# Performance work log

Measured on AMD Instinct MI355X. Metric: run time of the kernel, lower is better.

## Reference

```python
import jax, jax.numpy as jnp
import numpy as np

D = 512       # hidden_size (attention defaults hardcode 512)
N = 8         # num_heads
H = D // N    # depth per head = 64
FF = 2048     # FFN filter size (hardcoded)
EPS = 1e-6


def _layer_norm(x, gamma, beta):
    # matches functional layer_norm: biased variance, eps inside sqrt
    mean = jnp.mean(x, axis=-1, keepdims=True)
    var = jnp.mean((x - mean) ** 2, axis=-1, keepdims=True)
    return gamma * ((x - mean) / jnp.sqrt(var + EPS)) + beta


def setup_inputs() -> dict:
    key = jax.random.key(0)
    ks = jax.random.split(key, 12)
    B, S = 8, 1024
    s = lambda k, shape, scale: jax.random.normal(k, shape, jnp.float32) * scale
    return {
        "inputs": s(ks[0], (B, S, D), 1.0),
        "attention_bias": jnp.zeros((B, 1, 1, S), jnp.float32),
        "ln1_g": jnp.ones((D,), jnp.float32),
        "ln1_b": jnp.zeros((D,), jnp.float32),
        "wq": s(ks[1], (D, N, H), D ** -0.5),
        "wk": s(ks[2], (D, N, H), D ** -0.5),
        "wv": s(ks[3], (D, N, H), D ** -0.5),
        "wo": s(ks[4], (N, H, D), D ** -0.5),
        "ln2_g": jnp.ones((D,), jnp.float32),
        "ln2_b": jnp.zeros((D,), jnp.float32),
        "w1": s(ks[5], (D, FF), D ** -0.5),
        "b1": jnp.zeros((FF,), jnp.float32),
        "w2": s(ks[6], (FF, D), FF ** -0.5),
        "b2": jnp.zeros((D,), jnp.float32),
    }


def reference(inputs, attention_bias, ln1_g, ln1_b, wq, wk, wv, wo,
              ln2_g, ln2_b, w1, b1, w2, b2):
    # --- self-attention block (pre-LN, residual) ---
    y = _layer_norm(inputs, ln1_g, ln1_b)
    q = jnp.einsum('bsd,dnh->bsnh', y, wq) * (H ** -0.5)
    k = jnp.einsum('bsd,dnh->bsnh', y, wk)
    v = jnp.einsum('bsd,dnh->bsnh', y, wv)
    # logits[b,n,f,t] = sum_h k[b,t,n,h] * q[b,f,n,h]
    logits = jnp.einsum('btnh,bfnh->bnft', k, q) + attention_bias
    weights = jax.nn.softmax(logits, axis=3)
    attn = jnp.einsum('bnft,btnh->bfnh', weights, v)
    attn_out = jnp.einsum('bfnh,nhd->bfd', attn, wo)
    x = inputs + attn_out

    # --- FFN block (pre-LN, residual) ---
    y2 = _layer_norm(x, ln2_g, ln2_b)
    h = jax.nn.relu(jnp.einsum('bsd,df->bsf', y2, w1) + b1)
    ffn_out = jnp.einsum('bsf,fd->bsd', h, w2) + b2
    return x + ffn_out
```

## Files before the change

kernel.cpp:

```cpp
#include <hip/hip_runtime.h>
#include <stdint.h>

typedef unsigned short u16;
typedef __attribute__((ext_vector_type(8))) __bf16 bf16x8;
typedef __attribute__((ext_vector_type(2))) __bf16 bf16x2;
typedef __attribute__((ext_vector_type(4))) float f32x4;

__device__ __forceinline__ float bf2f(u16 u) {
    union { unsigned int i; float f; } c; c.i = ((unsigned int)u) << 16; return c.f;
}
__device__ __forceinline__ u16 f2bf_sw(float f) {
    union { float f; unsigned int i; } c; c.f = f;
    unsigned int u = c.i;
    u += 0x7FFFu + ((u >> 16) & 1u);
    return (u16)(u >> 16);
}
__device__ __forceinline__ unsigned f2bf2(float lo, float hi) {
#if __has_builtin(__builtin_amdgcn_cvt_pk_bf16_f32)
    union { bf16x2 v; unsigned u; } c;
    c.v = __builtin_amdgcn_cvt_pk_bf16_f32(lo, hi);
    return c.u;
#else
    return (unsigned)f2bf_sw(lo) | ((unsigned)f2bf_sw(hi) << 16);
#endif
}
__device__ __forceinline__ u16 f2bf(float f) {
#if __has_builtin(__builtin_amdgcn_cvt_pk_bf16_f32)
    return (u16)(f2bf2(f, 0.f) & 0xFFFFu);
#else
    return f2bf_sw(f);
#endif
}
__device__ __forceinline__ bool sniff_f32(const unsigned* probe) {
    return probe && ((*probe & 0xFFFFu) == 0u);
}
__device__ __forceinline__ float lde(const void* p, size_t i, bool isf32) {
    return isf32 ? ((const float*)p)[i] : bf2f(((const u16*)p)[i]);
}
__device__ __forceinline__ void g2lds16(const void* g, void* l) {
    __builtin_amdgcn_global_load_lds(
        (__attribute__((address_space(1))) void*)(uintptr_t)g,
        (__attribute__((address_space(3))) void*)(unsigned int)(uintptr_t)l,
        16, 0, 0);
}

__global__ void prep_weights(const void* __restrict__ wq, const void* __restrict__ wk,
                             const void* __restrict__ wv, const void* __restrict__ wo,
                             const void* __restrict__ w1, const void* __restrict__ w2,
                             u16* __restrict__ wqkvT, u16* __restrict__ woT,
                             u16* __restrict__ w1T, u16* __restrict__ w2T,
                             const unsigned* probe) {
    __shared__ u16 t[32][33];
    const bool isf32 = sniff_f32(probe);
    const int id = blockIdx.x;
    const void* src; u16* dst; int R, C, cb, rb; float scale = 1.f;
    if (id < 1024) {
        const int which = id >> 8, tl = id & 255;
        R = 512; C = 512; cb = (tl & 15) * 32; rb = (tl >> 4) * 32;
        if (which == 0)      { src = wq; dst = wqkvT;              scale = 0.18033688011112042f; }
        else if (which == 1) { src = wk; dst = wqkvT + 512 * 512; }
        else if (which == 2) { src = wv; dst = wqkvT + 1024 * 512; }
        else                 { src = wo; dst = woT; }
    } else if (id < 2048) {
        const int tl = id - 1024; src = w1; dst = w1T; R = 512; C = 2048;
        cb = (tl & 63) * 32; rb = (tl >> 6) * 32;
    } else {
        const int tl = id - 2048; src = w2; dst = w2T; R = 2048; C = 512;
        cb = (tl & 15) * 32; rb = (tl >> 4) * 32;
    }
    const int tx = threadIdx.x, ty = threadIdx.y;
#pragma unroll
    for (int i = 0; i < 4; i++)
        t[ty + i * 8][tx] = f2bf(lde(src, (size_t)(rb + ty + i * 8) * C + cb + tx, isf32));
    __syncthreads();
#pragma unroll
    for (int i = 0; i < 4; i++) {
        float v = bf2f(t[tx][ty + i * 8]) * scale;
        dst[(size_t)(cb + ty + i * 8) * R + rb + tx] = f2bf(v);
    }
}

__global__ __launch_bounds__(256) void ln_any(const void* __restrict__ x,
                                              const void* __restrict__ gw,
                                              const void* __restrict__ bw,
                                              u16* __restrict__ y,
                                              const unsigned* probe_x,
                                              const unsigned* probe_gb) {
    const bool xf32 = sniff_f32(probe_x);
    const bool gf32 = sniff_f32(probe_gb);
    const int lane = threadIdx.x & 63, wave = threadIdx.x >> 6;
    const int r = blockIdx.x * 4 + wave;
    union U8 { uint4 v; u16 s[8]; };
    float xs[8];
    if (xf32) {
        const float4* xr = (const float4*)((const float*)x + (size_t)r * 512 + lane * 8);
        float4 p0 = xr[0], p1 = xr[1];
        xs[0]=p0.x; xs[1]=p0.y; xs[2]=p0.z; xs[3]=p0.w;
        xs[4]=p1.x; xs[5]=p1.y; xs[6]=p1.z; xs[7]=p1.w;
    } else {
        U8 xu; xu.v = *(const uint4*)((const u16*)x + (size_t)r * 512 + lane * 8);
#pragma unroll
        for (int j = 0; j < 8; j++) xs[j] = bf2f(xu.s[j]);
    }
    float s1 = 0.f, s2 = 0.f;
#pragma unroll
    for (int j = 0; j < 8; j++) { s1 += xs[j]; s2 += xs[j] * xs[j]; }
#pragma unroll
    for (int d = 1; d < 64; d <<= 1) { s1 += __shfl_xor(s1, d); s2 += __shfl_xor(s2, d); }
    const float mean = s1 * (1.f / 512.f);
    const float var = s2 * (1.f / 512.f) - mean * mean;
    const float rstd = rsqrtf(var + 1e-6f);
    float gs[8], bs[8];
    if (gf32) {
        const float4* gr = (const float4*)((const float*)gw + lane * 8);
        const float4* br = (const float4*)((const float*)bw + lane * 8);
        float4 g0 = gr[0], g1 = gr[1], b0 = br[0], b1 = br[1];
        gs[0]=g0.x; gs[1]=g0.y; gs[2]=g0.z; gs[3]=g0.w; gs[4]=g1.x; gs[5]=g1.y; gs[6]=g1.z; gs[7]=g1.w;
        bs[0]=b0.x; bs[1]=b0.y; bs[2]=b0.z; bs[3]=b0.w; bs[4]=b1.x; bs[5]=b1.y; bs[6]=b1.z; bs[7]=b1.w;
    } else {
        U8 gu; gu.v = *(const uint4*)((const u16*)gw + lane * 8);
        U8 bu; bu.v = *(const uint4*)((const u16*)bw + lane * 8);
#pragma unroll
        for (int j = 0; j < 8; j++) { gs[j] = bf2f(gu.s[j]); bs[j] = bf2f(bu.s[j]); }
    }
    uint4 ov;
    float o[8];
#pragma unroll
    for (int j = 0; j < 8; j++) o[j] = gs[j] * ((xs[j] - mean) * rstd) + bs[j];
    ov.x = f2bf2(o[0], o[1]); ov.y = f2bf2(o[2], o[3]);
    ov.z = f2bf2(o[4], o[5]); ov.w = f2bf2(o[6], o[7]);
    *(uint4*)(y + (size_t)r * 512 + lane * 8) = ov;
}

template <int EPI, int TM>
__global__ __launch_bounds__(256, 2) void gemm_bt(const u16* __restrict__ A,
                                                  const u16* __restrict__ Bt,
                                                  const void* __restrict__ bias,
                                                  const void* __restrict__ res,
                                                  void* __restrict__ out,
                                                  u16* __restrict__ out2,
                                                  const unsigned* probe,
                                                  int M, int N, int K) {
    constexpr int ACH = TM / 16;
    constexpr int MI = TM / 32;
    __shared__ __align__(16) u16 lA[2][TM * 32];
    __shared__ __align__(16) u16 lB[2][128 * 32];
    const int tid = threadIdx.x, wave = tid >> 6, lane = tid & 63;
    const int m0 = blockIdx.x * TM, n0 = blockIdx.y * 128;
    const int wm = (wave >> 1) * (TM / 2), wn = (wave & 1) * 64;
    const int row = lane & 15, quad = lane >> 4;
    f32x4 acc[MI][4];
#pragma unroll
    for (int i = 0; i < MI; i++)
#pragma unroll
        for (int j = 0; j < 4; j++) acc[i][j] = (f32x4){0.f, 0.f, 0.f, 0.f};
    const u16* Ab = A + (size_t)m0 * K;
    const u16* Bb = Bt + (size_t)n0 * K;

    auto stage = [&](int buf, int k0) {
#pragma unroll
        for (int c = 0; c < (ACH + 8 + 3) / 4; c++) {
            const int ch = c * 4 + wave;
            if (ch < ACH) {
                const int e = ch * 64 + lane;
                const int r = e >> 2, col = (e & 3) * 8;
                g2lds16(Ab + (size_t)r * K + k0 + col, (char*)lA[buf] + ch * 1024);
            } else if (ch < ACH + 8) {
                const int c2 = ch - ACH;
                const int e = c2 * 64 + lane;
                const int r = e >> 2, col = (e & 3) * 8;
                g2lds16(Bb + (size_t)r * K + k0 + col, (char*)lB[buf] + c2 * 1024);
            }
        }
    };

    stage(0, 0);
    int cur = 0;
    for (int k0 = 0; k0 < K; k0 += 32) {
        __syncthreads();
        if (k0 + 32 < K) stage(cur ^ 1, k0 + 32);
        bf16x8 af[MI], bfr[4];
#pragma unroll
        for (int t = 0; t < MI; t++)
            af[t]  = *(const bf16x8*)(lA[cur] + (wm + t * 16 + row) * 32 + quad * 8);
#pragma unroll
        for (int t = 0; t < 4; t++)
            bfr[t] = *(const bf16x8*)(lB[cur] + (wn + t * 16 + row) * 32 + quad * 8);
#pragma unroll
        for (int i = 0; i < MI; i++)
#pragma unroll
            for (int j = 0; j < 4; j++)
                acc[i][j] = __builtin_amdgcn_mfma_f32_16x16x32_bf16(af[i], bfr[j], acc[i][j], 0, 0, 0);
        cur ^= 1;
    }
    const bool isf32 = sniff_f32(probe);
#pragma unroll
    for (int i = 0; i < MI; i++) {
        const int gm = m0 + wm + i * 16 + quad * 4;
#pragma unroll
        for (int j = 0; j < 4; j++) {
            const int gn = n0 + wn + j * 16 + row;
            float bv = 0.f;
            if (EPI == 2 || EPI == 3) bv = lde(bias, gn, isf32);
#pragma unroll
            for (int r = 0; r < 4; r++) {
                float v = acc[i][j][r];
                const int gmr = gm + r;
                size_t idx = (size_t)gmr * N + gn;
                if (EPI == 1) {
                    ((u16*)out)[idx] = f2bf(v + lde(res, idx, isf32));
                } else if (EPI == 2) {
                    v += bv;
                    ((u16*)out)[idx] = f2bf(v > 0.f ? v : 0.f);
                } else if (EPI == 3) {
                    v += bv + bf2f(((const u16*)res)[idx]);
                    if (isf32) ((float*)out)[idx] = v;
                    else       ((u16*)out)[idx] = f2bf(v);
                } else {
                    if (gn < 1024) {
                        ((u16*)out)[(size_t)gmr * 1024 + gn] = f2bf(v);
                    } else {
                        const int j2 = gn - 1024, n = j2 >> 6, h2 = j2 & 63;
                        const int b = gmr >> 10, t = gmr & 1023;
                        const int ut = t & 31, vt = ut & 15;
                        const int tP = (t & ~31) | ((vt >> 2) * 8 + ((ut >> 4) << 2) + (vt & 3));
                        out2[(((size_t)b * 8 + n) * 64 + h2) * 1024 + tP] = f2bf(v);
                    }
                }
            }
        }
    }
}

__global__ __launch_bounds__(256, 4) void attn_fused(const u16* __restrict__ qk,
                                                     const u16* __restrict__ vT,
                                                     const void* __restrict__ biasp,
                                                     u16* __restrict__ attn,
                                                     const unsigned* probe) {
    __shared__ __align__(16) u16 lQ[64 * 64];
    __shared__ __align__(16) u16 lK[128 * 64];
    __shared__ __align__(16) u16 lV[64 * 128];
    const bool isf32 = sniff_f32(probe);
    const int tid = threadIdx.x, wave = tid >> 6, lane = tid & 63;
    const int row = lane & 15, quad = lane >> 4;
    const int bn = blockIdx.x, b = bn >> 3, n = bn & 7;
    const int f0 = blockIdx.y * 64;
    const u16* Qg = qk + (size_t)(b * 1024 + f0) * 1024 + n * 64;
    const u16* Kg = qk + (size_t)(b * 1024) * 1024 + 512 + n * 64;
    const u16* Vg = vT + (size_t)bn * 65536;

#pragma unroll
    for (int j = 0; j < 2; j++) {
        const int ch = wave * 2 + j, e = ch * 64 + lane;
        const int rq = e >> 3, cq = ((e & 7) ^ (rq & 7)) * 8;
        g2lds16(Qg + (size_t)rq * 1024 + cq, (char*)lQ + ch * 1024);
    }
    __syncthreads();
    const int fr = wave * 16 + row;
    bf16x8 bq[2];
#pragma unroll
    for (int ks = 0; ks < 2; ks++)
        bq[ks] = *(const bf16x8*)(lQ + fr * 64 + (((ks * 4 + quad) ^ (fr & 7)) * 8));

    float l_i = 0.f;
    f32x4 oacc[4];
#pragma unroll
    for (int h = 0; h < 4; h++) oacc[h] = (f32x4){0.f, 0.f, 0.f, 0.f};

    for (int t0 = 0; t0 < 1024; t0 += 128) {
        __syncthreads();
#pragma unroll
        for (int j = 0; j < 4; j++) {
            const int ch = wave * 4 + j, e = ch * 64 + lane;
            const int rk = e >> 3, ck = ((e & 7) ^ (rk & 7)) * 8;
            g2lds16(Kg + (size_t)(t0 + rk) * 1024 + ck, (char*)lK + ch * 1024);
            const int rv = e >> 4, cv = ((e & 15) ^ (rv & 7)) * 8;
            g2lds16(Vg + (size_t)rv * 1024 + t0 + cv, (char*)lV + ch * 1024);
        }
        __syncthreads();
        f32x4 s[8];
#pragma unroll
        for (int nt = 0; nt < 8; nt++) s[nt] = (f32x4){0.f, 0.f, 0.f, 0.f};
#pragma unroll
        for (int nt = 0; nt < 8; nt++) {
            const int tr = nt * 16 + row;
#pragma unroll
            for (int ks = 0; ks < 2; ks++) {
                bf16x8 ak = *(const bf16x8*)(lK + tr * 64 + (((ks * 4 + quad) ^ (tr & 7)) * 8));
                s[nt] = __builtin_amdgcn_mfma_f32_16x16x32_bf16(ak, bq[ks], s[nt], 0, 0, 0);
            }
        }
#pragma unroll
        for (int nt = 0; nt < 8; nt++) {
            const size_t bidx = (size_t)b * 1024 + t0 + nt * 16 + quad * 4;
            float bv4[4];
            if (isf32) {
                float4 t4 = *(const float4*)((const float*)biasp + bidx);
                bv4[0] = t4.x; bv4[1] = t4.y; bv4[2] = t4.z; bv4[3] = t4.w;
            } else {
                union { uint2 v; u16 s[4]; } bu;
                bu.v = *(const uint2*)((const u16*)biasp + bidx);
#pragma unroll
                for (int r = 0; r < 4; r++) bv4[r] = bf2f(bu.s[r]);
            }
#pragma unroll
            for (int r = 0; r < 4; r++) {
                float p = __builtin_exp2f(fmaf(bv4[r], 1.4426950408889634f, s[nt][r]));
                s[nt][r] = p;
                l_i += p;
            }
        }
#pragma unroll
        for (int ks = 0; ks < 4; ks++) {
            union { unsigned u[4]; bf16x8 v8; } bb;
            bb.u[0] = f2bf2(s[ks * 2][0],     s[ks * 2][1]);
            bb.u[1] = f2bf2(s[ks * 2][2],     s[ks * 2][3]);
            bb.u[2] = f2bf2(s[ks * 2 + 1][0], s[ks * 2 + 1][1]);
            bb.u[3] = f2bf2(s[ks * 2 + 1][2], s[ks * 2 + 1][3]);
#pragma unroll
            for (int ht = 0; ht < 4; ht++) {
                const int vr = ht * 16 + row;
                bf16x8 av = *(const bf16x8*)(lV + vr * 128 + (((ks * 4 + quad) ^ (vr & 7)) * 8));
                oacc[ht] = __builtin_amdgcn_mfma_f32_16x16x32_bf16(av, bb.v8, oacc[ht], 0, 0, 0);
            }
        }
    }
    l_i += __shfl_xor(l_i, 16);
    l_i += __shfl_xor(l_i, 32);
    const float inv = 1.f / l_i;
    const int f = f0 + wave * 16 + row;
#pragma unroll
    for (int ht = 0; ht < 4; ht++) {
        uint2 ov;
        ov.x = f2bf2(oacc[ht][0] * inv, oacc[ht][1] * inv);
        ov.y = f2bf2(oacc[ht][2] * inv, oacc[ht][3] * inv);
        *(uint2*)(attn + (size_t)(b * 1024 + f) * 512 + n * 64 + ht * 16 + quad * 4) = ov;
    }
}

extern "C" void kernel_launch(void* const* d_in, const int* in_sizes, int n_in,
                              void* d_out, int out_size, void* d_ws, size_t ws_size,
                              hipStream_t stream) {
    const void* inp  = d_in[0];
    const void* ab   = d_in[1];
    const void* ln1g = d_in[2];
    const void* ln1b = d_in[3];
    const void* wq   = d_in[4];
    const void* wk   = d_in[5];
    const void* wv   = d_in[6];
    const void* wo   = d_in[7];
    const void* ln2g = d_in[8];
    const void* ln2b = d_in[9];
    const void* w1   = d_in[10];
    const void* b1   = d_in[11];
    const void* w2   = d_in[12];
    const void* b2   = d_in[13];
    const unsigned* probe = (const unsigned*)d_in[2];

    char* ws = (char*)d_ws;
    size_t off = 0;
    auto alloc = [&](size_t bytes) -> void* { void* p = ws + off; off += bytes; return p; };
    u16* wqkvT = (u16*)alloc(1536 * 512 * 2);
    u16* woT   = (u16*)alloc(512 * 512 * 2);
    u16* w1T   = (u16*)alloc(2048 * 512 * 2);
    u16* w2T   = (u16*)alloc(512 * 2048 * 2);
    u16* ybuf  = (u16*)alloc((size_t)8192 * 512 * 2);
    u16* qk    = (u16*)alloc((size_t)8192 * 1024 * 2);
    u16* vT    = (u16*)alloc((size_t)64 * 64 * 1024 * 2);
    u16* attn  = (u16*)alloc((size_t)8192 * 512 * 2);
    u16* xbf   = (u16*)alloc((size_t)8192 * 512 * 2);
    u16* hbuf  = qk;

    prep_weights<<<3072, dim3(32, 8), 0, stream>>>(wq, wk, wv, wo, w1, w2,
                                                   wqkvT, woT, w1T, w2T, probe);
    ln_any<<<2048, 256, 0, stream>>>(inp, ln1g, ln1b, ybuf, probe, probe);
    gemm_bt<4, 128><<<dim3(64, 12), 256, 0, stream>>>(ybuf, wqkvT, nullptr, nullptr, qk, vT, nullptr, 8192, 1536, 512);
    attn_fused<<<dim3(64, 16), 256, 0, stream>>>(qk, vT, ab, attn, probe);
    gemm_bt<1, 64><<<dim3(128, 4), 256, 0, stream>>>(attn, woT, nullptr, inp, xbf, nullptr, probe, 8192, 512, 512);
    ln_any<<<2048, 256, 0, stream>>>(xbf, ln2g, ln2b, ybuf, nullptr, probe);
    gemm_bt<2, 128><<<dim3(64, 16), 256, 0, stream>>>(ybuf, w1T, b1, nullptr, hbuf, nullptr, probe, 8192, 2048, 512);
    gemm_bt<3, 64><<<dim3(128, 4), 256, 0, stream>>>(hbuf, w2T, b2, xbf, (u16*)d_out, nullptr, probe, 8192, 512, 2048);
}
```

Baseline: 253.5 us.

## Split attention over key dimension into two halves with separate merge kernel

The attention kernel now splits the 1024 keys into two halves via a third grid dimension, doubling block count. Each half writes unnormalized partial outputs and row sums, which a new merge kernel combines and normalizes. It also shrinks the K/V tiles to 64 keys, loads Q straight from global memory, and raises the occupancy hint so more blocks fit per CU. The cost is an extra kernel launch, extra global traffic for the partial buffers, and a second bf16 rounding of the unnormalized partials.

```diff
diff --git a/kernel.cpp b/kernel.cpp
--- a/kernel.cpp
+++ b/kernel.cpp
@@ -232,66 +232,62 @@
     }
 }
 
-__global__ __launch_bounds__(256, 4) void attn_fused(const u16* __restrict__ qk,
+__global__ __launch_bounds__(256, 7) void attn_fused(const u16* __restrict__ qk,
                                                      const u16* __restrict__ vT,
                                                      const void* __restrict__ biasp,
-                                                     u16* __restrict__ attn,
+                                                     u16* __restrict__ op0,
+                                                     u16* __restrict__ op1,
+                                                     float* __restrict__ lpart,
                                                      const unsigned* probe) {
-    __shared__ __align__(16) u16 lQ[64 * 64];
-    __shared__ __align__(16) u16 lK[128 * 64];
-    __shared__ __align__(16) u16 lV[64 * 128];
+    __shared__ __align__(16) u16 lK[64 * 64];
+    __shared__ __align__(16) u16 lV[64 * 64];
     const bool isf32 = sniff_f32(probe);
     const int tid = threadIdx.x, wave = tid >> 6, lane = tid & 63;
     const int row = lane & 15, quad = lane >> 4;
+    const int g0 = (quad ^ (row & 7)) * 8;
     const int bn = blockIdx.x, b = bn >> 3, n = bn & 7;
     const int f0 = blockIdx.y * 64;
+    const int z = blockIdx.z, ts = z * 512;
     const u16* Qg = qk + (size_t)(b * 1024 + f0) * 1024 + n * 64;
     const u16* Kg = qk + (size_t)(b * 1024) * 1024 + 512 + n * 64;
     const u16* Vg = vT + (size_t)bn * 65536;
 
-#pragma unroll
-    for (int j = 0; j < 2; j++) {
-        const int ch = wave * 2 + j, e = ch * 64 + lane;
-        const int rq = e >> 3, cq = ((e & 7) ^ (rq & 7)) * 8;
-        g2lds16(Qg + (size_t)rq * 1024 + cq, (char*)lQ + ch * 1024);
-    }
-    __syncthreads();
-    const int fr = wave * 16 + row;
     bf16x8 bq[2];
-#pragma unroll
-    for (int ks = 0; ks < 2; ks++)
-        bq[ks] = *(const bf16x8*)(lQ + fr * 64 + (((ks * 4 + quad) ^ (fr & 7)) * 8));
+    {
+        const u16* qrow = Qg + (size_t)(wave * 16 + row) * 1024;
+        bq[0] = *(const bf16x8*)(qrow + quad * 8);
+        bq[1] = *(const bf16x8*)(qrow + (4 + quad) * 8);
+    }
+
+    auto stageKV = [&](int t0) {
+#pragma unroll
+        for (int j = 0; j < 2; j++) {
+            const int ch = wave * 2 + j, e = ch * 64 + lane;
+            const int rk = e >> 3, ck = ((e & 7) ^ (rk & 7)) * 8;
+            g2lds16(Kg + (size_t)(t0 + rk) * 1024 + ck, (char*)lK + ch * 1024);
+            g2lds16(Vg + (size_t)rk * 1024 + t0 + ck, (char*)lV + ch * 1024);
+        }
+    };
 
     float l_i = 0.f;
     f32x4 oacc[4];
 #pragma unroll
     for (int h = 0; h < 4; h++) oacc[h] = (f32x4){0.f, 0.f, 0.f, 0.f};
 
-    for (int t0 = 0; t0 < 1024; t0 += 128) {
-        __syncthreads();
-#pragma unroll
-        for (int j = 0; j < 4; j++) {
-            const int ch = wave * 4 + j, e = ch * 64 + lane;
-            const int rk = e >> 3, ck = ((e & 7) ^ (rk & 7)) * 8;
-            g2lds16(Kg + (size_t)(t0 + rk) * 1024 + ck, (char*)lK + ch * 1024);
-            const int rv = e >> 4, cv = ((e & 15) ^ (rv & 7)) * 8;
-            g2lds16(Vg + (size_t)rv * 1024 + t0 + cv, (char*)lV + ch * 1024);
-        }
-        __syncthreads();
-        f32x4 s[8];
-#pragma unroll
-        for (int nt = 0; nt < 8; nt++) s[nt] = (f32x4){0.f, 0.f, 0.f, 0.f};
-#pragma unroll
-        for (int nt = 0; nt < 8; nt++) {
+    auto compute = [&](int t0) {
+        f32x4 s[4];
+#pragma unroll
+        for (int nt = 0; nt < 4; nt++) s[nt] = (f32x4){0.f, 0.f, 0.f, 0.f};
+#pragma unroll
+        for (int nt = 0; nt < 4; nt++) {
             const int tr = nt * 16 + row;
-#pragma unroll
-            for (int ks = 0; ks < 2; ks++) {
-                bf16x8 ak = *(const bf16x8*)(lK + tr * 64 + (((ks * 4 + quad) ^ (tr & 7)) * 8));
-                s[nt] = __builtin_amdgcn_mfma_f32_16x16x32_bf16(ak, bq[ks], s[nt], 0, 0, 0);
-            }
-        }
-#pragma unroll
-        for (int nt = 0; nt < 8; nt++) {
+            bf16x8 ak0 = *(const bf16x8*)(lK + tr * 64 + g0);
+            s[nt] = __builtin_amdgcn_mfma_f32_16x16x32_bf16(ak0, bq[0], s[nt], 0, 0, 0);
+            bf16x8 ak1 = *(const bf16x8*)(lK + tr * 64 + (g0 ^ 32));
+            s[nt] = __builtin_amdgcn_mfma_f32_16x16x32_bf16(ak1, bq[1], s[nt], 0, 0, 0);
+        }
+#pragma unroll
+        for (int nt = 0; nt < 4; nt++) {
             const size_t bidx = (size_t)b * 1024 + t0 + nt * 16 + quad * 4;
             float bv4[4];
             if (isf32) {
@@ -311,7 +307,7 @@
             }
         }
 #pragma unroll
-        for (int ks = 0; ks < 4; ks++) {
+        for (int ks = 0; ks < 2; ks++) {
             union { unsigned u[4]; bf16x8 v8; } bb;
             bb.u[0] = f2bf2(s[ks * 2][0],     s[ks * 2][1]);
             bb.u[1] = f2bf2(s[ks * 2][2],     s[ks * 2][3]);
@@ -319,23 +315,57 @@
             bb.u[3] = f2bf2(s[ks * 2 + 1][2], s[ks * 2 + 1][3]);
 #pragma unroll
             for (int ht = 0; ht < 4; ht++) {
-                const int vr = ht * 16 + row;
-                bf16x8 av = *(const bf16x8*)(lV + vr * 128 + (((ks * 4 + quad) ^ (vr & 7)) * 8));
+                bf16x8 av = *(const bf16x8*)(lV + (ht * 16 + row) * 64 + (g0 ^ (ks * 32)));
                 oacc[ht] = __builtin_amdgcn_mfma_f32_16x16x32_bf16(av, bb.v8, oacc[ht], 0, 0, 0);
             }
         }
-    }
+    };
+
+    stageKV(ts);
+    __syncthreads();
+    compute(ts);
+    for (int t0 = ts + 64; t0 < ts + 512; t0 += 64) {
+        __syncthreads();
+        stageKV(t0);
+        __syncthreads();
+        compute(t0);
+    }
+
     l_i += __shfl_xor(l_i, 16);
     l_i += __shfl_xor(l_i, 32);
-    const float inv = 1.f / l_i;
     const int f = f0 + wave * 16 + row;
+    if (quad == 0) lpart[((size_t)z * 64 + bn) * 1024 + f] = l_i;
+    u16* op = z ? op1 : op0;
 #pragma unroll
     for (int ht = 0; ht < 4; ht++) {
         uint2 ov;
-        ov.x = f2bf2(oacc[ht][0] * inv, oacc[ht][1] * inv);
-        ov.y = f2bf2(oacc[ht][2] * inv, oacc[ht][3] * inv);
-        *(uint2*)(attn + (size_t)(b * 1024 + f) * 512 + n * 64 + ht * 16 + quad * 4) = ov;
-    }
+        ov.x = f2bf2(oacc[ht][0], oacc[ht][1]);
+        ov.y = f2bf2(oacc[ht][2], oacc[ht][3]);
+        *(uint2*)(op + (size_t)(b * 1024 + f) * 512 + n * 64 + ht * 16 + quad * 4) = ov;
+    }
+}
+
+__global__ __launch_bounds__(256) void attn_merge(const u16* __restrict__ op0,
+                                                  const u16* __restrict__ op1,
+                                                  const float* __restrict__ lpart,
+                                                  u16* __restrict__ attn) {
+    const int lane = threadIdx.x & 63, wave = threadIdx.x >> 6;
+    const int r = blockIdx.x * 4 + wave;
+    const int b = r >> 10, f = r & 1023, n = lane >> 3;
+    const float l0 = lpart[((size_t)(b * 8 + n)) * 1024 + f];
+    const float l1 = lpart[((size_t)(64 + b * 8 + n)) * 1024 + f];
+    const float inv = 1.f / (l0 + l1);
+    const size_t idx = (size_t)r * 512 + lane * 8;
+    union U8 { uint4 v; u16 s[8]; } a0, a1;
+    a0.v = *(const uint4*)(op0 + idx);
+    a1.v = *(const uint4*)(op1 + idx);
+    float o[8];
+#pragma unroll
+    for (int j = 0; j < 8; j++) o[j] = (bf2f(a0.s[j]) + bf2f(a1.s[j])) * inv;
+    uint4 ov;
+    ov.x = f2bf2(o[0], o[1]); ov.y = f2bf2(o[2], o[3]);
+    ov.z = f2bf2(o[4], o[5]); ov.w = f2bf2(o[6], o[7]);
+    *(uint4*)(attn + idx) = ov;
 }
 
 extern "C" void kernel_launch(void* const* d_in, const int* in_sizes, int n_in,
@@ -369,13 +399,15 @@
     u16* vT    = (u16*)alloc((size_t)64 * 64 * 1024 * 2);
     u16* attn  = (u16*)alloc((size_t)8192 * 512 * 2);
     u16* xbf   = (u16*)alloc((size_t)8192 * 512 * 2);
+    float* lpart = (float*)alloc((size_t)2 * 64 * 1024 * 4);
     u16* hbuf  = qk;
 
     prep_weights<<<3072, dim3(32, 8), 0, stream>>>(wq, wk, wv, wo, w1, w2,
                                                    wqkvT, woT, w1T, w2T, probe);
     ln_any<<<2048, 256, 0, stream>>>(inp, ln1g, ln1b, ybuf, probe, probe);
     gemm_bt<4, 128><<<dim3(64, 12), 256, 0, stream>>>(ybuf, wqkvT, nullptr, nullptr, qk, vT, nullptr, 8192, 1536, 512);
-    attn_fused<<<dim3(64, 16), 256, 0, stream>>>(qk, vT, ab, attn, probe);
+    attn_fused<<<dim3(64, 16, 2), 256, 0, stream>>>(qk, vT, ab, ybuf, xbf, lpart, probe);
+    attn_merge<<<2048, 256, 0, stream>>>(ybuf, xbf, lpart, attn);
     gemm_bt<1, 64><<<dim3(128, 4), 256, 0, stream>>>(attn, woT, nullptr, inp, xbf, nullptr, probe, 8192, 512, 512);
     ln_any<<<2048, 256, 0, stream>>>(xbf, ln2g, ln2b, ybuf, nullptr, probe);
     gemm_bt<2, 128><<<dim3(64, 16), 256, 0, stream>>>(ybuf, w1T, b1, nullptr, hbuf, nullptr, probe, 8192, 2048, 512);
```

Result: slower. 285.0 us (+12.5%).

## Split attention key range across two wave groups with double-buffered KV pipeline

Applied to the files above, without the earlier changes.

The attention kernel moves to 512 threads, where two groups of four waves each process alternating 32-key chunks. K/V tiles are double-buffered in LDS with async global-to-LDS loads issued ahead and partial vmcnt waits, and the bias row is staged once in LDS. Q is loaded straight into registers, and the two groups' partial outputs and sums are combined through LDS at the end. This aims to overlap memory loads with MFMA work and raise occupancy, at the cost of smaller per-iteration tiles, more barriers and a final reduction step.

```diff
diff --git a/kernel.cpp b/kernel.cpp
--- a/kernel.cpp
+++ b/kernel.cpp
@@ -42,6 +42,11 @@
         (__attribute__((address_space(1))) void*)(uintptr_t)g,
         (__attribute__((address_space(3))) void*)(unsigned int)(uintptr_t)l,
         16, 0, 0);
+}
+__device__ __forceinline__ void fence_bar() {
+    __builtin_amdgcn_sched_barrier(0);
+    __builtin_amdgcn_s_barrier();
+    __builtin_amdgcn_sched_barrier(0);
 }
 
 __global__ void prep_weights(const void* __restrict__ wq, const void* __restrict__ wk,
@@ -232,109 +237,144 @@
     }
 }
 
-__global__ __launch_bounds__(256, 4) void attn_fused(const u16* __restrict__ qk,
+__global__ __launch_bounds__(512, 8) void attn_fused(const u16* __restrict__ qk,
                                                      const u16* __restrict__ vT,
                                                      const void* __restrict__ biasp,
                                                      u16* __restrict__ attn,
                                                      const unsigned* probe) {
-    __shared__ __align__(16) u16 lQ[64 * 64];
-    __shared__ __align__(16) u16 lK[128 * 64];
-    __shared__ __align__(16) u16 lV[64 * 128];
+    __shared__ __align__(16) char smem[36864];
+    u16* lKb = (u16*)smem;
+    u16* lVb = (u16*)(smem + 16384);
+    char* lB = smem + 32768;
     const bool isf32 = sniff_f32(probe);
     const int tid = threadIdx.x, wave = tid >> 6, lane = tid & 63;
+    const int wid = wave & 3, grp = wave >> 2;
     const int row = lane & 15, quad = lane >> 4;
+    const int g0 = (quad ^ (row & 7)) * 8;
+    const int gV = (quad ^ (row & 3)) * 8;
     const int bn = blockIdx.x, b = bn >> 3, n = bn & 7;
     const int f0 = blockIdx.y * 64;
     const u16* Qg = qk + (size_t)(b * 1024 + f0) * 1024 + n * 64;
     const u16* Kg = qk + (size_t)(b * 1024) * 1024 + 512 + n * 64;
     const u16* Vg = vT + (size_t)bn * 65536;
 
-#pragma unroll
-    for (int j = 0; j < 2; j++) {
-        const int ch = wave * 2 + j, e = ch * 64 + lane;
-        const int rq = e >> 3, cq = ((e & 7) ^ (rq & 7)) * 8;
-        g2lds16(Qg + (size_t)rq * 1024 + cq, (char*)lQ + ch * 1024);
-    }
-    __syncthreads();
-    const int fr = wave * 16 + row;
+    auto stageKV = [&](int slot, int t0) {
+        const int rk = wid * 8 + (lane >> 3);
+        const int ck = ((lane & 7) ^ (rk & 7)) * 8;
+        g2lds16(Kg + (size_t)(t0 + rk) * 1024 + ck, (char*)(lKb + slot * 2048) + wid * 1024);
+        const int rv = wid * 16 + (lane >> 2);
+        const int cv = ((lane & 3) ^ (rv & 3)) * 8;
+        g2lds16(Vg + (size_t)rv * 1024 + t0 + cv, (char*)(lVb + slot * 2048) + wid * 1024);
+    };
+
     bf16x8 bq[2];
-#pragma unroll
-    for (int ks = 0; ks < 2; ks++)
-        bq[ks] = *(const bf16x8*)(lQ + fr * 64 + (((ks * 4 + quad) ^ (fr & 7)) * 8));
+    {
+        const u16* qrow = Qg + (size_t)(wid * 16 + row) * 1024;
+        bq[0] = *(const bf16x8*)(qrow + quad * 8);
+        bq[1] = *(const bf16x8*)(qrow + (4 + quad) * 8);
+    }
+    if (grp == 0) {
+        if (isf32)
+            g2lds16((const float*)biasp + (size_t)b * 1024 + wid * 256 + lane * 4, lB + wid * 1024);
+        else if (wid < 2)
+            g2lds16((const u16*)biasp + (size_t)b * 1024 + wid * 512 + lane * 8, lB + wid * 1024);
+    }
+    stageKV(grp * 2,     grp * 32);
+    stageKV(grp * 2 + 1, (2 + grp) * 32);
+    asm volatile("s_waitcnt vmcnt(0)" ::: "memory");
+    fence_bar();
 
     float l_i = 0.f;
     f32x4 oacc[4];
 #pragma unroll
     for (int h = 0; h < 4; h++) oacc[h] = (f32x4){0.f, 0.f, 0.f, 0.f};
 
-    for (int t0 = 0; t0 < 1024; t0 += 128) {
-        __syncthreads();
-#pragma unroll
-        for (int j = 0; j < 4; j++) {
-            const int ch = wave * 4 + j, e = ch * 64 + lane;
-            const int rk = e >> 3, ck = ((e & 7) ^ (rk & 7)) * 8;
-            g2lds16(Kg + (size_t)(t0 + rk) * 1024 + ck, (char*)lK + ch * 1024);
-            const int rv = e >> 4, cv = ((e & 15) ^ (rv & 7)) * 8;
-            g2lds16(Vg + (size_t)rv * 1024 + t0 + cv, (char*)lV + ch * 1024);
-        }
-        __syncthreads();
-        f32x4 s[8];
-#pragma unroll
-        for (int nt = 0; nt < 8; nt++) s[nt] = (f32x4){0.f, 0.f, 0.f, 0.f};
-#pragma unroll
-        for (int nt = 0; nt < 8; nt++) {
+    auto compute = [&](int slot, int t0) {
+        const u16* lKc = lKb + slot * 2048;
+        const u16* lVc = lVb + slot * 2048;
+        f32x4 s2[2];
+        s2[0] = (f32x4){0.f, 0.f, 0.f, 0.f};
+        s2[1] = (f32x4){0.f, 0.f, 0.f, 0.f};
+#pragma unroll
+        for (int nt = 0; nt < 2; nt++) {
             const int tr = nt * 16 + row;
-#pragma unroll
-            for (int ks = 0; ks < 2; ks++) {
-                bf16x8 ak = *(const bf16x8*)(lK + tr * 64 + (((ks * 4 + quad) ^ (tr & 7)) * 8));
-                s[nt] = __builtin_amdgcn_mfma_f32_16x16x32_bf16(ak, bq[ks], s[nt], 0, 0, 0);
-            }
-        }
-#pragma unroll
-        for (int nt = 0; nt < 8; nt++) {
-            const size_t bidx = (size_t)b * 1024 + t0 + nt * 16 + quad * 4;
+            bf16x8 ak0 = *(const bf16x8*)(lKc + tr * 64 + g0);
+            s2[nt] = __builtin_amdgcn_mfma_f32_16x16x32_bf16(ak0, bq[0], s2[nt], 0, 0, 0);
+            bf16x8 ak1 = *(const bf16x8*)(lKc + tr * 64 + (g0 ^ 32));
+            s2[nt] = __builtin_amdgcn_mfma_f32_16x16x32_bf16(ak1, bq[1], s2[nt], 0, 0, 0);
+        }
+#pragma unroll
+        for (int nt = 0; nt < 2; nt++) {
+            const int tl = t0 + nt * 16 + quad * 4;
             float bv4[4];
             if (isf32) {
-                float4 t4 = *(const float4*)((const float*)biasp + bidx);
+                float4 t4 = *(const float4*)((const float*)lB + tl);
                 bv4[0] = t4.x; bv4[1] = t4.y; bv4[2] = t4.z; bv4[3] = t4.w;
             } else {
                 union { uint2 v; u16 s[4]; } bu;
-                bu.v = *(const uint2*)((const u16*)biasp + bidx);
+                bu.v = *(const uint2*)((const u16*)lB + tl);
 #pragma unroll
                 for (int r = 0; r < 4; r++) bv4[r] = bf2f(bu.s[r]);
             }
 #pragma unroll
             for (int r = 0; r < 4; r++) {
-                float p = __builtin_exp2f(fmaf(bv4[r], 1.4426950408889634f, s[nt][r]));
-                s[nt][r] = p;
+                float p = __builtin_exp2f(fmaf(bv4[r], 1.4426950408889634f, s2[nt][r]));
+                s2[nt][r] = p;
                 l_i += p;
             }
         }
-#pragma unroll
-        for (int ks = 0; ks < 4; ks++) {
-            union { unsigned u[4]; bf16x8 v8; } bb;
-            bb.u[0] = f2bf2(s[ks * 2][0],     s[ks * 2][1]);
-            bb.u[1] = f2bf2(s[ks * 2][2],     s[ks * 2][3]);
-            bb.u[2] = f2bf2(s[ks * 2 + 1][0], s[ks * 2 + 1][1]);
-            bb.u[3] = f2bf2(s[ks * 2 + 1][2], s[ks * 2 + 1][3]);
-#pragma unroll
-            for (int ht = 0; ht < 4; ht++) {
-                const int vr = ht * 16 + row;
-                bf16x8 av = *(const bf16x8*)(lV + vr * 128 + (((ks * 4 + quad) ^ (vr & 7)) * 8));
-                oacc[ht] = __builtin_amdgcn_mfma_f32_16x16x32_bf16(av, bb.v8, oacc[ht], 0, 0, 0);
-            }
-        }
-    }
-    l_i += __shfl_xor(l_i, 16);
-    l_i += __shfl_xor(l_i, 32);
-    const float inv = 1.f / l_i;
-    const int f = f0 + wave * 16 + row;
-#pragma unroll
-    for (int ht = 0; ht < 4; ht++) {
-        uint2 ov;
-        ov.x = f2bf2(oacc[ht][0] * inv, oacc[ht][1] * inv);
-        ov.y = f2bf2(oacc[ht][2] * inv, oacc[ht][3] * inv);
-        *(uint2*)(attn + (size_t)(b * 1024 + f) * 512 + n * 64 + ht * 16 + quad * 4) = ov;
+        union { unsigned u[4]; bf16x8 v8; } bb;
+        bb.u[0] = f2bf2(s2[0][0], s2[0][1]);
+        bb.u[1] = f2bf2(s2[0][2], s2[0][3]);
+        bb.u[2] = f2bf2(s2[1][0], s2[1][1]);
+        bb.u[3] = f2bf2(s2[1][2], s2[1][3]);
+#pragma unroll
+        for (int ht = 0; ht < 4; ht++) {
+            bf16x8 av = *(const bf16x8*)(lVc + (ht * 16 + row) * 32 + gV);
+            oacc[ht] = __builtin_amdgcn_mfma_f32_16x16x32_bf16(av, bb.v8, oacc[ht], 0, 0, 0);
+        }
+    };
+
+#pragma unroll 1
+    for (int s = 0; s < 15; s++) {
+        compute(grp * 2 + (s & 1), (2 * s + grp) * 32);
+        fence_bar();
+        if (s <= 13) {
+            stageKV(grp * 2 + (s & 1), (2 * (s + 2) + grp) * 32);
+            asm volatile("s_waitcnt vmcnt(2)" ::: "memory");
+        } else {
+            asm volatile("s_waitcnt vmcnt(0)" ::: "memory");
+        }
+        fence_bar();
+    }
+    compute(grp * 2 + 1, (30 + grp) * 32);
+
+    __syncthreads();
+    float* scr = (float*)smem;
+    float* scrL = scr + 4608;
+    if (grp == 1) {
+#pragma unroll
+        for (int ht = 0; ht < 4; ht++)
+            *(f32x4*)(scr + wid * 1152 + (ht * 64 + lane) * 4) = oacc[ht];
+        scrL[wid * 64 + lane] = l_i;
+    }
+    __syncthreads();
+    if (grp == 0) {
+#pragma unroll
+        for (int ht = 0; ht < 4; ht++)
+            oacc[ht] += *(const f32x4*)(scr + wid * 1152 + (ht * 64 + lane) * 4);
+        l_i += scrL[wid * 64 + lane];
+        l_i += __shfl_xor(l_i, 16);
+        l_i += __shfl_xor(l_i, 32);
+        const float inv = 1.f / l_i;
+        const int f = f0 + wid * 16 + row;
+#pragma unroll
+        for (int ht = 0; ht < 4; ht++) {
+            uint2 ov;
+            ov.x = f2bf2(oacc[ht][0] * inv, oacc[ht][1] * inv);
+            ov.y = f2bf2(oacc[ht][2] * inv, oacc[ht][3] * inv);
+            *(uint2*)(attn + (size_t)(b * 1024 + f) * 512 + n * 64 + ht * 16 + quad * 4) = ov;
+        }
     }
 }
 
@@ -375,7 +415,7 @@
                                                    wqkvT, woT, w1T, w2T, probe);
     ln_any<<<2048, 256, 0, stream>>>(inp, ln1g, ln1b, ybuf, probe, probe);
     gemm_bt<4, 128><<<dim3(64, 12), 256, 0, stream>>>(ybuf, wqkvT, nullptr, nullptr, qk, vT, nullptr, 8192, 1536, 512);
-    attn_fused<<<dim3(64, 16), 256, 0, stream>>>(qk, vT, ab, attn, probe);
+    attn_fused<<<dim3(64, 16), 512, 0, stream>>>(qk, vT, ab, attn, probe);
     gemm_bt<1, 64><<<dim3(128, 4), 256, 0, stream>>>(attn, woT, nullptr, inp, xbf, nullptr, probe, 8192, 512, 512);
     ln_any<<<2048, 256, 0, stream>>>(xbf, ln2g, ln2b, ybuf, nullptr, probe);
     gemm_bt<2, 128><<<dim3(64, 16), 256, 0, stream>>>(ybuf, w1T, b1, nullptr, hbuf, nullptr, probe, 8192, 2048, 512);
```

New measurement: 251.2 us. About the same (-0.9%).
